# Optimization experiments

Measured on AMD Instinct MI355X. Metric: run time of the kernel, lower is better.

Reference implementation:

```python
import jax, jax.numpy as jnp
import numpy as np

B, N, E = 16, 1000, 16000        # graphs, nodes/graph, edges/graph
H1, C1 = 8, 128                  # conv1 heads, per-head channels (hidden_size)
EMB, HID = 64, 128               # embed_size, mlp hidden_size


def gat_conv(x, ei, W, att_src, att_dst, bias, heads, concat):
    """PyG GATConv (eval mode, self-loops already in ei). x: [Ntot, Fin]."""
    Ntot = x.shape[0]
    C = W.shape[1] // heads
    h = (x @ W).reshape(Ntot, heads, C)                  # [Ntot, H, C]
    a_src = jnp.einsum('nhc,hc->nh', h, att_src)          # [Ntot, H]
    a_dst = jnp.einsum('nhc,hc->nh', h, att_dst)
    src, dst = ei[0], ei[1]
    alpha = jax.nn.leaky_relu(a_src[src] + a_dst[dst], 0.2)   # [Etot, H]
    # segment softmax over destination nodes (every node has a self loop)
    amax = jax.ops.segment_max(alpha, dst, num_segments=Ntot)
    ea = jnp.exp(alpha - amax[dst])
    denom = jax.ops.segment_sum(ea, dst, num_segments=Ntot)
    alpha = ea / denom[dst]
    msg = h[src] * alpha[:, :, None]                      # [Etot, H, C]
    out = jax.ops.segment_sum(msg, dst, num_segments=Ntot)   # [Ntot, H, C]
    out = out.reshape(Ntot, heads * C) if concat else out.mean(axis=1)
    return out + bias


def setup_inputs():
    key = jax.random.key(0)
    k = jax.random.split(key, 16)
    g = lambda kk, sh: (jax.random.normal(kk, sh, jnp.float32) * 0.1)
    return {
        'actions': jax.random.normal(k[0], (B, N, 2), jnp.float32),
        'node_features': jax.random.normal(k[1], (B, 1, N), jnp.float32),
        'edge_index': jax.random.randint(k[2], (B, 2, E), 0, N, dtype=jnp.int32),
        # conv1: GATConv(3, C1, heads=H1, concat=True)
        'W1': g(k[3], (3, H1 * C1)),
        'att_src1': g(k[4], (H1, C1)),
        'att_dst1': g(k[5], (H1, C1)),
        'b1': g(k[6], (H1 * C1,)),
        # conv2: GATConv(H1*C1, EMB, heads=1, concat=False)
        'W2': g(k[7], (H1 * C1, EMB)),
        'att_src2': g(k[8], (1, EMB)),
        'att_dst2': g(k[9], (1, EMB)),
        'b2': g(k[10], (EMB,)),
        # MLP head
        'mlp_w1': g(k[11], (N * EMB, HID)),
        'mlp_b1': jnp.zeros((HID,), jnp.float32),
        'mlp_w2': g(k[12], (HID, HID)),
        'mlp_b2': jnp.zeros((HID,), jnp.float32),
        'out_w': g(k[13], (HID, N)),
        'out_b': jnp.zeros((N,), jnp.float32),
    }


def reference(actions, node_features, edge_index, W1, att_src1, att_dst1, b1,
              W2, att_src2, att_dst2, b2, mlp_w1, mlp_b1, mlp_w2, mlp_b2,
              out_w, out_b):
    Bn, _, Nn = node_features.shape
    nf = node_features.astype(jnp.float32).squeeze(1)                 # [B, N]
    x = jnp.stack([actions[:, :, 0], actions[:, :, 1], nf], axis=2)   # [B, N, 3]
    x = x.reshape(Bn * Nn, 3)
    # batch-offset edge index, then faithful row-major reshape to [2, B*E]
    ei = (edge_index + (jnp.arange(Bn) * Nn)[:, None, None]).reshape(2, -1)
    loops = jnp.broadcast_to(jnp.arange(Bn * Nn)[None, :], (2, Bn * Nn))
    ei = jnp.concatenate([ei, loops], axis=1)
    # eval mode: dropouts are no-ops
    x = jax.nn.elu(gat_conv(x, ei, W1, att_src1, att_dst1, b1, H1, True))
    x = jax.nn.elu(gat_conv(x, ei, W2, att_src2, att_dst2, b2, 1, False))
    x = x.reshape(Bn, Nn * EMB)
    x = jax.nn.relu(x @ mlp_w1 + mlp_b1)
    x = jax.nn.relu(x @ mlp_w2 + mlp_b2)
    return jax.nn.sigmoid(x @ out_w + out_b)                          # [B, N]
```

## Files before the change

kernel.cpp:

```cpp
#include <hip/hip_runtime.h>
#include <math.h>

#define NB 16
#define NN 1000
#define NT 16000
#define NE 16000
#define EBASE 256000
#define ETOT 272000
#define F1 1024
#define EMB 64
#define HID 128
#define NREP 8
#define CAP 96
#define PBASE 0xAAAAAAAAu
#define LIGHT_N 8000

typedef unsigned short ushort_t;
typedef unsigned int uint_t;
typedef __attribute__((ext_vector_type(8))) _Float16 half8;
typedef __attribute__((ext_vector_type(4))) _Float16 half4_;
typedef __attribute__((ext_vector_type(4))) float float4_;
typedef __attribute__((ext_vector_type(2))) float float2_;
typedef __attribute__((ext_vector_type(2))) uint_t uint2_;

__device__ __forceinline__ int src_of(const int* ei, int j) {
    if (j < EBASE) return ei[j] + (j / 32000) * 1000;
    return j - EBASE;
}
__device__ __forceinline__ int dst_of(const int* ei, int j) {
    if (j < EBASE) return ei[EBASE + j] + (8 + j / 32000) * 1000;
    return j - EBASE;
}

__device__ __forceinline__ float lrelu02(float r) { return r >= 0.f ? r : 0.2f * r; }
__device__ __forceinline__ float elu1(float v)    { return v > 0.f ? v : __expf(v) - 1.f; }
__device__ __forceinline__ ushort_t f2h(float f) {
    _Float16 h = (_Float16)f;
    union { _Float16 h; ushort_t u; } c; c.h = h; return c.u;
}

__global__ __launch_bounds__(256) void k_prepfill(
    const float* __restrict__ actions, const float* __restrict__ nf,
    const float* __restrict__ W1, const float* __restrict__ as1w, const float* __restrict__ ad1w,
    const float* __restrict__ W2, const int* __restrict__ ei,
    float* __restrict__ srcpack, float* __restrict__ ad1,
    ushort_t* __restrict__ w2f, int* __restrict__ cnt, int* __restrict__ esrc) {
    __shared__ float tile[64][65];
    __shared__ float was[24], wad[24];
    int bid = blockIdx.x, t = threadIdx.x;

    if (bid < 63) {
        if (t < 24) {
            int k = t / 8, h = t % 8;
            float ss = 0.f, dd = 0.f;
            for (int c = 0; c < 128; ++c) {
                float w = W1[k * F1 + h * 128 + c];
                ss += w * as1w[h * 128 + c];
                dd += w * ad1w[h * 128 + c];
            }
            was[t] = ss; wad[t] = dd;
        }
        __syncthreads();
        int n = bid * 256 + t;
        if (n < NT) {
            float x0 = actions[n * 2 + 0];
            float x1v = actions[n * 2 + 1];
            float x2v = nf[n];
            float4_ a03, a47;
            #pragma unroll
            for (int h = 0; h < 4; ++h) {
                a03[h] = x0 * was[h] + x1v * was[8 + h] + x2v * was[16 + h];
                a47[h] = x0 * was[4 + h] + x1v * was[12 + h] + x2v * was[20 + h];
            }
            float4_ xv = {x0, x1v, x2v, 0.f};
            float* sp = srcpack + (size_t)n * 16;
            *(float4_*)(sp)      = a03;
            *(float4_*)(sp + 4)  = a47;
            *(float4_*)(sp + 8)  = xv;
            #pragma unroll
            for (int h = 0; h < 8; ++h)
                ad1[n * 8 + h] = x0 * wad[h] + x1v * wad[8 + h] + x2v * wad[16 + h];
        }
    } else if (bid < 79) {
        int k0 = (bid - 63) * 64;
        int c = t & 63, g = t >> 6;
        for (int r = g; r < 64; r += 4)
            tile[r][c] = W2[(size_t)(k0 + r) * 64 + c];
        __syncthreads();
        for (int q = t; q < 512; q += 256) {
            int t4 = q >> 7, ksl = (q >> 6) & 1, l8 = q & 63;
            int kg = l8 >> 4, mrow = l8 & 15;
            int n = t4 * 16 + mrow;
            int kloc = ksl * 32 + kg * 8;
            size_t base = (((size_t)t4 * 32 + (k0 >> 5) + ksl) * 64 + l8) * 8;
            #pragma unroll
            for (int j = 0; j < 8; ++j)
                w2f[base + j] = f2h(tile[kloc + j][n]);
        }
    } else {
        int j = (bid - 79) * 256 + t;
        if (j < ETOT) {
            if (j < EBASE + LIGHT_N && j >= EBASE) {
            } else {
                int dv = dst_of(ei, j);
                uint_t old = (uint_t)atomicAdd(&cnt[dv], 1);
                int slot = (int)(old - PBASE);
                if (slot >= 0 && slot < CAP)
                    esrc[(size_t)dv * CAP + slot] = src_of(ei, j);
            }
        }
    }
}

__global__ __launch_bounds__(256) void k_conv1h2(
    const int* __restrict__ cnt, const int* __restrict__ esrc,
    const float* __restrict__ srcpack, const float* __restrict__ ad1,
    const float* __restrict__ W1, const float* __restrict__ b1,
    const ushort_t* __restrict__ w2f,
    const float* __restrict__ as2w, const float* __restrict__ ad2w,
    ushort_t* __restrict__ h2h, float* __restrict__ a2s, float* __restrict__ a2d) {
    __shared__ ushort_t x1t[16][1032];
    __shared__ float smb[16][8][3];
    __shared__ float a2p[4][16][2];
    int t = threadIdx.x, wave = t >> 6, lane = t & 63;

    float4_ w0 = *(const float4_*)(W1 + t * 4);
    float4_ w1r = *(const float4_*)(W1 + F1 + t * 4);
    float4_ w2r = *(const float4_*)(W1 + 2 * F1 + t * 4);
    float4_ bb = *(const float4_*)(b1 + t * 4);

    int g = lane >> 4, lg = lane & 15, eslot = lg >> 3, h = lg & 7;
    int nd0 = wave * 4 + g;
    int d = blockIdx.x * 16 + nd0;

    if (d < LIGHT_N) {
        if (eslot == 0) {
            const float* sp = srcpack + (size_t)d * 16;
            smb[nd0][h][0] = sp[8];
            smb[nd0][h][1] = sp[9];
            smb[nd0][h][2] = sp[10];
        }
    } else {
        int cn = (int)((uint_t)cnt[d] - PBASE);
        cn = (cn < CAP) ? cn : CAP;
        const int* ep = esrc + (size_t)d * CAP;
        float adv = ad1[d * 8 + h];
        float den = 0.f, s0 = 0.f, s1 = 0.f, s2 = 0.f;
        {
            int e = eslot;
            int sNext = (e < cn) ? ep[e] : 0;
            for (; e < cn; e += 2) {
                int s = sNext;
                if (e + 2 < cn) sNext = ep[e + 2];
                const float* sp = srcpack + (size_t)s * 16;
                float av = sp[h];
                float ea = __expf(lrelu02(av + adv));
                den += ea; s0 += ea * sp[8]; s1 += ea * sp[9]; s2 += ea * sp[10];
            }
        }
        den += __shfl_xor(den, 8, 64);
        s0  += __shfl_xor(s0, 8, 64);
        s1  += __shfl_xor(s1, 8, 64);
        s2  += __shfl_xor(s2, 8, 64);
        if (eslot == 0) {
            float inv = 1.f / den;
            smb[nd0][h][0] = s0 * inv;
            smb[nd0][h][1] = s1 * inv;
            smb[nd0][h][2] = s2 * inv;
        }
    }
    __syncthreads();

    int hh = t >> 5;
    #pragma unroll 4
    for (int nd = 0; nd < 16; ++nd) {
        float c0 = smb[nd][hh][0], c1 = smb[nd][hh][1], c2 = smb[nd][hh][2];
        float v0 = c0 * w0.x + c1 * w1r.x + c2 * w2r.x + bb.x;
        float v1 = c0 * w0.y + c1 * w1r.y + c2 * w2r.y + bb.y;
        float v2 = c0 * w0.z + c1 * w1r.z + c2 * w2r.z + bb.z;
        float v3 = c0 * w0.w + c1 * w1r.w + c2 * w2r.w + bb.w;
        v0 = elu1(v0); v1 = elu1(v1); v2 = elu1(v2); v3 = elu1(v3);
        uint2_ pk;
        pk.x = (uint_t)f2h(v0) | ((uint_t)f2h(v1) << 16);
        pk.y = (uint_t)f2h(v2) | ((uint_t)f2h(v3) << 16);
        *(uint2_*)(&x1t[nd][t * 4]) = pk;
    }
    __syncthreads();

    int mrow = lane & 15, kg = lane >> 4;
    const ushort_t* bp = w2f + ((size_t)wave * 32 * 64 + lane) * 8;
    float4_ acc = {0.f, 0.f, 0.f, 0.f};
    #pragma unroll 8
    for (int ks = 0; ks < 32; ++ks) {
        half8 a = *(const half8*)(&x1t[mrow][kg * 8 + ks * 32]);
        half8 b = *(const half8*)(bp + (size_t)ks * 512);
        acc = __builtin_amdgcn_mfma_f32_16x16x32_f16(a, b, acc, 0, 0, 0);
    }
    int row0 = blockIdx.x * 16;
    #pragma unroll
    for (int r = 0; r < 4; ++r)
        h2h[(size_t)(row0 + kg * 4 + r) * EMB + wave * 16 + mrow] = f2h(acc[r]);

    float sw = as2w[wave * 16 + mrow], dw = ad2w[wave * 16 + mrow];
    float ps[4], pd[4];
    #pragma unroll
    for (int r = 0; r < 4; ++r) { ps[r] = acc[r] * sw; pd[r] = acc[r] * dw; }
    #pragma unroll
    for (int st = 1; st < 16; st <<= 1) {
        #pragma unroll
        for (int r = 0; r < 4; ++r) {
            ps[r] += __shfl_xor(ps[r], st, 64);
            pd[r] += __shfl_xor(pd[r], st, 64);
        }
    }
    if (mrow == 0) {
        #pragma unroll
        for (int r = 0; r < 4; ++r) {
            a2p[wave][kg * 4 + r][0] = ps[r];
            a2p[wave][kg * 4 + r][1] = pd[r];
        }
    }
    __syncthreads();
    if (t < 16) {
        float ss = a2p[0][t][0] + a2p[1][t][0] + a2p[2][t][0] + a2p[3][t][0];
        float dd = a2p[0][t][1] + a2p[1][t][1] + a2p[2][t][1] + a2p[3][t][1];
        a2s[row0 + t] = ss; a2d[row0 + t] = dd;
    }
}

__global__ __launch_bounds__(512) void k_conv2mlp1(
    const int* __restrict__ cnt, const int* __restrict__ esrc, const ushort_t* __restrict__ h2h,
    const float* __restrict__ a2s, const float* __restrict__ a2d, const float* __restrict__ b2,
    const float* __restrict__ w1, float* __restrict__ y1rep) {
    __shared__ float x2s[EMB * NB];
    __shared__ float y1p[4 * NB * HID];
    int t = threadIdx.x;
    int wave = t >> 6, lane = t & 63;
    int n = blockIdx.x;
    int eg = lane >> 4, c4 = (lane & 15) * 4;

    {
        int b = wave;
        int d = b * NN + n;
        if (eg == 0) {
            half4_ hv = *(const half4_*)(h2h + (size_t)d * EMB + c4);
            #pragma unroll
            for (int q = 0; q < 4; ++q)
                x2s[(c4 + q) * NB + b] = elu1((float)hv[q] + b2[c4 + q]);
        }
    }

    {
        int b = 8 + wave;
        int d = b * NN + n;
        int cn = (int)((uint_t)cnt[d] - PBASE);
        cn = (cn < CAP) ? cn : CAP;
        const int* ep = esrc + (size_t)d * CAP;
        float adv = a2d[d];
        float den = 0.f;
        float4_ acc = {0.f, 0.f, 0.f, 0.f};
        int e = eg;
        int sNext = (e < cn) ? ep[e] : 0;
        for (; e < cn; e += 4) {
            int s = sNext;
            if (e + 4 < cn) sNext = ep[e + 4];
            float ea = __expf(lrelu02(a2s[s] + adv));
            half4_ hv = *(const half4_*)(h2h + (size_t)s * EMB + c4);
            den += ea;
            acc.x += ea * (float)hv.x; acc.y += ea * (float)hv.y;
            acc.z += ea * (float)hv.z; acc.w += ea * (float)hv.w;
        }
        #pragma unroll
        for (int st = 16; st < 64; st <<= 1) {
            den   += __shfl_xor(den, st, 64);
            acc.x += __shfl_xor(acc.x, st, 64);
            acc.y += __shfl_xor(acc.y, st, 64);
            acc.z += __shfl_xor(acc.z, st, 64);
            acc.w += __shfl_xor(acc.w, st, 64);
        }
        if (eg == 0) {
            float inv = 1.f / den;
            #pragma unroll
            for (int q = 0; q < 4; ++q)
                x2s[(c4 + q) * NB + b] = elu1(acc[q] * inv + b2[c4 + q]);
        }
    }
    __syncthreads();

    int j = t & 127, kq = t >> 7;
    float am[NB];
    #pragma unroll
    for (int b = 0; b < NB; ++b) am[b] = 0.f;
    const float* wp = w1 + ((size_t)n * EMB + kq * 16) * HID + j;
    #pragma unroll 4
    for (int kk = 0; kk < 16; ++kk) {
        float w = wp[(size_t)kk * HID];
        const float* xr = x2s + (kq * 16 + kk) * NB;
        float4_ xb0 = *(const float4_*)(xr);
        float4_ xb1 = *(const float4_*)(xr + 4);
        float4_ xb2 = *(const float4_*)(xr + 8);
        float4_ xb3 = *(const float4_*)(xr + 12);
        am[0] += xb0.x * w; am[1] += xb0.y * w; am[2] += xb0.z * w; am[3] += xb0.w * w;
        am[4] += xb1.x * w; am[5] += xb1.y * w; am[6] += xb1.z * w; am[7] += xb1.w * w;
        am[8] += xb2.x * w; am[9] += xb2.y * w; am[10] += xb2.z * w; am[11] += xb2.w * w;
        am[12] += xb3.x * w; am[13] += xb3.y * w; am[14] += xb3.z * w; am[15] += xb3.w * w;
    }
    #pragma unroll
    for (int b = 0; b < NB; ++b)
        y1p[(kq * NB + b) * HID + j] = am[b];
    __syncthreads();

    float* yp = y1rep + (size_t)(blockIdx.x & (NREP - 1)) * (NB * HID);
    #pragma unroll
    for (int i = 0; i < 4; ++i) {
        int idx = i * 512 + t;
        float v = (y1p[idx] + y1p[NB * HID + idx])
                + (y1p[2 * NB * HID + idx] + y1p[3 * NB * HID + idx]);
        atomicAdd(&yp[idx], v);
    }
}

__global__ __launch_bounds__(256) void k_tail(
    const float* __restrict__ y1rep, const float* __restrict__ mb1,
    const float* __restrict__ mw2, const float* __restrict__ mb2,
    const float* __restrict__ ow, const float* __restrict__ ob,
    float* __restrict__ out) {
    __shared__ float y1[NB * HID];
    __shared__ float y2s[NB * HID];
    __shared__ float oacc[16][16][17];
    int t = threadIdx.x;

    for (int idx = t; idx < NB * HID; idx += 256) {
        float s = 0.f;
        #pragma unroll
        for (int r = 0; r < NREP; ++r)
            s += y1rep[(size_t)r * (NB * HID) + idx];
        y1[idx] = fmaxf(s + mb1[idx & 127], 0.f);
    }
    __syncthreads();

    {
        int j = t & 127, bh = t >> 7;
        float acc[8];
        #pragma unroll
        for (int q = 0; q < 8; ++q) acc[q] = mb2[j];
        #pragma unroll 4
        for (int k = 0; k < HID; ++k) {
            float w = mw2[k * HID + j];
            #pragma unroll
            for (int q = 0; q < 8; ++q)
                acc[q] += y1[(bh + 2 * q) * HID + k] * w;
        }
        #pragma unroll
        for (int q = 0; q < 8; ++q)
            y2s[(bh + 2 * q) * HID + j] = fmaxf(acc[q], 0.f);
    }
    __syncthreads();

    int nl = t & 15, jg = t >> 4;
    int n = blockIdx.x * 16 + nl;
    float acc[NB];
    #pragma unroll
    for (int b = 0; b < NB; ++b) acc[b] = 0.f;
    if (n < NN) {
        #pragma unroll
        for (int jj = 0; jj < 8; ++jj) {
            int j = jg * 8 + jj;
            float w = ow[j * NN + n];
            #pragma unroll
            for (int b = 0; b < NB; ++b) acc[b] += y2s[b * HID + j] * w;
        }
    }
    #pragma unroll
    for (int b = 0; b < NB; ++b) oacc[jg][nl][b] = acc[b];
    __syncthreads();
    int b = t >> 4, nl2 = t & 15;
    float s = 0.f;
    #pragma unroll
    for (int q = 0; q < 16; ++q) s += oacc[q][nl2][b];
    int n2 = blockIdx.x * 16 + nl2;
    if (n2 < NN)
        out[b * NN + n2] = 1.f / (1.f + __expf(-(s + ob[n2])));
}

extern "C" void kernel_launch(void* const* d_in, const int* in_sizes, int n_in,
                              void* d_out, int out_size, void* d_ws, size_t ws_size,
                              hipStream_t stream) {
    const float* actions = (const float*)d_in[0];
    const float* nf      = (const float*)d_in[1];
    const int*   ei      = (const int*)d_in[2];
    const float* W1      = (const float*)d_in[3];
    const float* as1w    = (const float*)d_in[4];
    const float* ad1w    = (const float*)d_in[5];
    const float* b1      = (const float*)d_in[6];
    const float* W2      = (const float*)d_in[7];
    const float* as2w    = (const float*)d_in[8];
    const float* ad2w    = (const float*)d_in[9];
    const float* b2      = (const float*)d_in[10];
    const float* mw1     = (const float*)d_in[11];
    const float* mb1     = (const float*)d_in[12];
    const float* mw2     = (const float*)d_in[13];
    const float* mb2     = (const float*)d_in[14];
    const float* ow      = (const float*)d_in[15];
    const float* ob      = (const float*)d_in[16];
    float* out = (float*)d_out;

    float* f = (float*)d_ws;
    float* srcpack = f;  f += (size_t)NT * 16;
    float* ad1   = f;  f += NT * 8;
    float* a2s   = f;  f += NT;
    float* a2d   = f;  f += NT;
    float* y1rep = f;  f += (size_t)NREP * NB * HID;
    ushort_t* h2h = (ushort_t*)f;
    ushort_t* w2f = h2h + (size_t)NT * EMB;
    int* ip = (int*)(w2f + 65536);
    int* cnt  = ip; ip += NT;
    int* esrc = ip; ip += (size_t)NT * CAP;

    k_prepfill<<<1142, 256, 0, stream>>>(actions, nf, W1, as1w, ad1w, W2, ei,
                                         srcpack, ad1, w2f, cnt, esrc);
    k_conv1h2<<<NT / 16, 256, 0, stream>>>(cnt, esrc, srcpack, ad1, W1, b1, w2f,
                                           as2w, ad2w, h2h, a2s, a2d);
    k_conv2mlp1<<<NN, 512, 0, stream>>>(cnt, esrc, h2h, a2s, a2d, b2, mw1, y1rep);
    k_tail<<<64, 256, 0, stream>>>(y1rep, mb1, mw2, mb2, ow, ob, out);
}
```

Baseline: 175.7 us.

## Build CSR adjacency per graph with LDS counting sort instead of global atomic buckets

Replaces the fixed-capacity per-node edge buckets, which relied on global atomics and a poisoned counter base, with a per-graph CSR build. One block per heavy graph counts destinations in LDS, runs a block-wide prefix scan to get offsets, and scatters sources with LDS atomics. Consumer kernels now read cnt and off arrays instead of fixed CAP-strided slots. This removes the global atomic contention and the CAP truncation, but concentrates the edge work in only 8 blocks, each processing 32000 edges serially.

```diff
diff --git a/kernel.cpp b/kernel.cpp
--- a/kernel.cpp
+++ b/kernel.cpp
@@ -6,14 +6,13 @@
 #define NT 16000
 #define NE 16000
 #define EBASE 256000
-#define ETOT 272000
 #define F1 1024
 #define EMB 64
 #define HID 128
 #define NREP 8
-#define CAP 96
 #define PBASE 0xAAAAAAAAu
 #define LIGHT_N 8000
+#define CHN 33000
 
 typedef unsigned short ushort_t;
 typedef unsigned int uint_t;
@@ -23,15 +22,6 @@
 typedef __attribute__((ext_vector_type(2))) float float2_;
 typedef __attribute__((ext_vector_type(2))) uint_t uint2_;
 
-__device__ __forceinline__ int src_of(const int* ei, int j) {
-    if (j < EBASE) return ei[j] + (j / 32000) * 1000;
-    return j - EBASE;
-}
-__device__ __forceinline__ int dst_of(const int* ei, int j) {
-    if (j < EBASE) return ei[EBASE + j] + (8 + j / 32000) * 1000;
-    return j - EBASE;
-}
-
 __device__ __forceinline__ float lrelu02(float r) { return r >= 0.f ? r : 0.2f * r; }
 __device__ __forceinline__ float elu1(float v)    { return v > 0.f ? v : __expf(v) - 1.f; }
 __device__ __forceinline__ ushort_t f2h(float f) {
@@ -39,17 +29,21 @@
     union { _Float16 h; ushort_t u; } c; c.h = h; return c.u;
 }
 
-__global__ __launch_bounds__(256) void k_prepfill(
+__global__ __launch_bounds__(512) void k_prepfill(
     const float* __restrict__ actions, const float* __restrict__ nf,
     const float* __restrict__ W1, const float* __restrict__ as1w, const float* __restrict__ ad1w,
     const float* __restrict__ W2, const int* __restrict__ ei,
     float* __restrict__ srcpack, float* __restrict__ ad1,
-    ushort_t* __restrict__ w2f, int* __restrict__ cnt, int* __restrict__ esrc) {
+    ushort_t* __restrict__ w2f, int* __restrict__ cnt, int* __restrict__ off,
+    int* __restrict__ esrc) {
     __shared__ float tile[64][65];
     __shared__ float was[24], wad[24];
+    __shared__ int cnt1k[1000];
+    __shared__ int off1k[1000];
+    __shared__ int wsum[8];
     int bid = blockIdx.x, t = threadIdx.x;
 
-    if (bid < 63) {
+    if (bid < 32) {
         if (t < 24) {
             int k = t / 8, h = t % 8;
             float ss = 0.f, dd = 0.f;
@@ -61,7 +55,7 @@
             was[t] = ss; wad[t] = dd;
         }
         __syncthreads();
-        int n = bid * 256 + t;
+        int n = bid * 512 + t;
         if (n < NT) {
             float x0 = actions[n * 2 + 0];
             float x1v = actions[n * 2 + 1];
@@ -81,13 +75,14 @@
             for (int h = 0; h < 8; ++h)
                 ad1[n * 8 + h] = x0 * wad[h] + x1v * wad[8 + h] + x2v * wad[16 + h];
         }
-    } else if (bid < 79) {
-        int k0 = (bid - 63) * 64;
+    } else if (bid < 48) {
+        int k0 = (bid - 32) * 64;
         int c = t & 63, g = t >> 6;
-        for (int r = g; r < 64; r += 4)
+        for (int r = g; r < 64; r += 8)
             tile[r][c] = W2[(size_t)(k0 + r) * 64 + c];
         __syncthreads();
-        for (int q = t; q < 512; q += 256) {
+        {
+            int q = t;
             int t4 = q >> 7, ksl = (q >> 6) & 1, l8 = q & 63;
             int kg = l8 >> 4, mrow = l8 & 15;
             int n = t4 * 16 + mrow;
@@ -98,22 +93,64 @@
                 w2f[base + j] = f2h(tile[kloc + j][n]);
         }
     } else {
-        int j = (bid - 79) * 256 + t;
-        if (j < ETOT) {
-            if (j < EBASE + LIGHT_N && j >= EBASE) {
-            } else {
-                int dv = dst_of(ei, j);
-                uint_t old = (uint_t)atomicAdd(&cnt[dv], 1);
-                int slot = (int)(old - PBASE);
-                if (slot >= 0 && slot < CAP)
-                    esrc[(size_t)dv * CAP + slot] = src_of(ei, j);
-            }
+        int bb = bid - 48;
+        const int* dstp = ei + EBASE + bb * 32000;
+        const int* srcp = ei + bb * 32000;
+        int base = bb * CHN;
+
+        for (int m = t; m < 1000; m += 512) cnt1k[m] = 1;
+        __syncthreads();
+        for (int jj = t; jj < 32000; jj += 512)
+            atomicAdd(&cnt1k[dstp[jj]], 1);
+        __syncthreads();
+
+        int i2 = t * 2;
+        int a  = (i2 < 1000) ? cnt1k[i2] : 0;
+        int b2 = (i2 + 1 < 1000) ? cnt1k[i2 + 1] : 0;
+        int s = a + b2;
+        int lane = t & 63, w = t >> 6;
+        int sc = s;
+        #pragma unroll
+        for (int st = 1; st < 64; st <<= 1) {
+            int o = __shfl_up(sc, st, 64);
+            if (lane >= st) sc += o;
+        }
+        if (lane == 63) wsum[w] = sc;
+        __syncthreads();
+        if (t == 0) {
+            int acc = 0;
+            #pragma unroll
+            for (int k = 0; k < 8; ++k) { int x = wsum[k]; wsum[k] = acc; acc += x; }
+        }
+        __syncthreads();
+        int excl = wsum[w] + sc - s;
+        if (i2 < 1000) {
+            off1k[i2] = excl;
+            int d = (8 + bb) * 1000 + i2;
+            cnt[d] = a; off[d] = base + excl;
+        }
+        if (i2 + 1 < 1000) {
+            off1k[i2 + 1] = excl + a;
+            int d = (8 + bb) * 1000 + i2 + 1;
+            cnt[d] = b2; off[d] = base + excl + a;
+        }
+        __syncthreads();
+
+        for (int m = t; m < 1000; m += 512) {
+            cnt1k[m] = 1;
+            esrc[base + off1k[m]] = (8 + bb) * 1000 + m;
+        }
+        __syncthreads();
+        for (int jj = t; jj < 32000; jj += 512) {
+            int dl = dstp[jj];
+            int sl = atomicAdd(&cnt1k[dl], 1);
+            esrc[base + off1k[dl] + sl] = srcp[jj] + bb * 1000;
         }
     }
 }
 
 __global__ __launch_bounds__(256) void k_conv1h2(
-    const int* __restrict__ cnt, const int* __restrict__ esrc,
+    const int* __restrict__ cnt, const int* __restrict__ off, const int* __restrict__ esrc,
     const float* __restrict__ srcpack, const float* __restrict__ ad1,
     const float* __restrict__ W1, const float* __restrict__ b1,
     const ushort_t* __restrict__ w2f,
@@ -141,9 +178,8 @@
             smb[nd0][h][2] = sp[10];
         }
     } else {
-        int cn = (int)((uint_t)cnt[d] - PBASE);
-        cn = (cn < CAP) ? cn : CAP;
-        const int* ep = esrc + (size_t)d * CAP;
+        int cn = cnt[d];
+        const int* ep = esrc + off[d];
         float adv = ad1[d * 8 + h];
         float den = 0.f, s0 = 0.f, s1 = 0.f, s2 = 0.f;
         {
@@ -229,7 +265,8 @@
 }
 
 __global__ __launch_bounds__(512) void k_conv2mlp1(
-    const int* __restrict__ cnt, const int* __restrict__ esrc, const ushort_t* __restrict__ h2h,
+    const int* __restrict__ cnt, const int* __restrict__ off, const int* __restrict__ esrc,
+    const ushort_t* __restrict__ h2h,
     const float* __restrict__ a2s, const float* __restrict__ a2d, const float* __restrict__ b2,
     const float* __restrict__ w1, float* __restrict__ y1rep) {
     __shared__ float x2s[EMB * NB];
@@ -253,9 +290,8 @@
     {
         int b = 8 + wave;
         int d = b * NN + n;
-        int cn = (int)((uint_t)cnt[d] - PBASE);
-        cn = (cn < CAP) ? cn : CAP;
-        const int* ep = esrc + (size_t)d * CAP;
+        int cn = cnt[d];
+        const int* ep = esrc + off[d];
         float adv = a2d[d];
         float den = 0.f;
         float4_ acc = {0.f, 0.f, 0.f, 0.f};
@@ -415,12 +451,13 @@
     ushort_t* w2f = h2h + (size_t)NT * EMB;
     int* ip = (int*)(w2f + 65536);
     int* cnt  = ip; ip += NT;
-    int* esrc = ip; ip += (size_t)NT * CAP;
-
-    k_prepfill<<<1142, 256, 0, stream>>>(actions, nf, W1, as1w, ad1w, W2, ei,
-                                         srcpack, ad1, w2f, cnt, esrc);
-    k_conv1h2<<<NT / 16, 256, 0, stream>>>(cnt, esrc, srcpack, ad1, W1, b1, w2f,
+    int* offb = ip; ip += NT;
+    int* esrc = ip; ip += 8 * CHN;
+
+    k_prepfill<<<56, 512, 0, stream>>>(actions, nf, W1, as1w, ad1w, W2, ei,
+                                       srcpack, ad1, w2f, cnt, offb, esrc);
+    k_conv1h2<<<NT / 16, 256, 0, stream>>>(cnt, offb, esrc, srcpack, ad1, W1, b1, w2f,
                                            as2w, ad2w, h2h, a2s, a2d);
-    k_conv2mlp1<<<NN, 512, 0, stream>>>(cnt, esrc, h2h, a2s, a2d, b2, mw1, y1rep);
+    k_conv2mlp1<<<NN, 512, 0, stream>>>(cnt, offb, esrc, h2h, a2s, a2d, b2, mw1, y1rep);
     k_tail<<<64, 256, 0, stream>>>(y1rep, mb1, mw2, mb2, ow, ob, out);
 }
```

Result: slower. 227.6 us (+29.5%).
